# Optimization experiments

Hardware: AMD Instinct MI355X
Metric: run time of the kernel (lower is better)

The kernel has to match this reference:

```python
import jax, jax.numpy as jnp
import numpy as np

B, T, D = 128, 256, 1024  # batch, output_length (unroll steps), hidden size


def setup_inputs() -> dict:
    key = jax.random.key(0)
    k1, k2, k3 = jax.random.split(key, 3)
    scale = 0.02  # keep gates out of deep saturation
    return {
        "x": jax.random.normal(k1, (B, 1, D), dtype=jnp.float32),
        "kernel": jax.random.normal(k2, (D, 3 * D), dtype=jnp.float32) * scale,
        "rec_kernel": jax.random.normal(k3, (D, 3 * D), dtype=jnp.float32) * scale,
        "bias": jnp.zeros((3 * D,), dtype=jnp.float32),
        "output_length": T,
    }


def _gru_cell(x, h, kernel, rec_kernel, bias):
    # Classic GRU (Keras reset_after=False): gates from input and recurrent paths.
    gx = x @ kernel + bias            # [B, 3D]
    gh = h @ rec_kernel               # [B, 3D]
    xz, xr, xh = jnp.split(gx, 3, axis=-1)
    hz, hr, hh = jnp.split(gh, 3, axis=-1)
    z = jax.nn.sigmoid(xz + hz)       # update gate
    r = jax.nn.sigmoid(xr + hr)       # reset gate
    h_cand = jnp.tanh(xh + r * hh)
    return z * h + (1.0 - z) * h_cand


def reference(x, kernel, rec_kernel, bias, output_length):
    # RecursiveUnroll: feed the cell its own output, seeded by x, state init zeros.
    x0 = x[:, 0, :]                   # [B, D]
    h0 = jnp.zeros_like(x0)

    def step(carry, _):
        xt, ht = carry
        h_new = _gru_cell(xt, ht, kernel, rec_kernel, bias)
        # cell output == new state; it is both next input and next state
        return (h_new, h_new), h_new

    _, ys = jax.lax.scan(step, (x0, h0), None, length=output_length - 1)  # [T-1, B, D]
    out = jnp.concatenate([x0[None], ys], axis=0)  # [T, B, D]; first slot is the seed x
    return jnp.transpose(out, (1, 0, 2))           # [B, T, D]
```

## Files before the change

### kernel.cpp

```cpp
#include <hip/hip_runtime.h>
#include <hip/hip_bf16.h>

typedef short s16x8 __attribute__((ext_vector_type(8)));
typedef float f32x4 __attribute__((ext_vector_type(4)));

#define B_  128
#define T_  256
#define D_  1024

#define WPACK_BYTES (6144u * 2048u)
#define HBUF_BYTES  (128u * 1024u * 2u)
#define HA_OFF      (WPACK_BYTES)
#define HB_OFF      (HA_OFF + HBUF_BYTES)
#define SLOTS_OFF   (HB_OFF + HBUF_BYTES)
#define EPOCH_OFF   (SLOTS_OFF + 256u * 64u)
#define WS_NEEDED   (EPOCH_OFF + 8u * 64u)

static __device__ __forceinline__ float sigm_f(float x) {
  float e = __builtin_amdgcn_exp2f(-1.4426950408889634f * x);
  return __builtin_amdgcn_rcpf(1.0f + e);
}
static __device__ __forceinline__ float tanh_f(float x) {
  float e = __builtin_amdgcn_exp2f(-2.8853900817779268f * x);
  return 2.0f * __builtin_amdgcn_rcpf(1.0f + e) - 1.0f;
}
static __device__ __forceinline__ unsigned short f2bf(float f) {
  return __builtin_bit_cast(unsigned short, __float2bfloat16(f));
}
static __device__ __forceinline__ s16x8 ldg_coh(const char* p) {
  s16x8 v;
  asm volatile("global_load_dwordx4 %0, %1, off sc0 sc1" : "=v"(v) : "v"(p));
  return v;
}
static __device__ __forceinline__ void stg_coh(char* p, s16x8 v) {
  asm volatile("global_store_dwordx4 %0, %1, off sc0 sc1" :: "v"(p), "v"(v) : "memory");
}
static __device__ __forceinline__ unsigned hoff(int b, int k) {
  unsigned bb = (unsigned)b >> 6, mt = ((unsigned)b >> 4) & 3u, r = (unsigned)b & 15u;
  unsigned kk = (unsigned)k >> 5, g = ((unsigned)k >> 3) & 3u, k0 = (unsigned)k & 7u;
  return (((((bb * 32u + kk) * 4u + mt) * 4u + g) * 16u + r) * 8u + k0) * 2u;
}

extern "C" __global__ __launch_bounds__(256)
void gru_prepass(const float* __restrict__ x, const float* __restrict__ Wk,
                 const float* __restrict__ Wr, float* __restrict__ out,
                 char* __restrict__ ws) {
  const int W = blockIdx.x, tid = threadIdx.x;
  if (W < 3072) {
    const int v = W * 4 + (tid >> 6);
    const int lane = tid & 63;
    const int cb = v % 96, gk = v / 96;
    const int c = cb * 64 + lane;
    const float* src = (c < 3072) ? (Wk + c) : (Wr + (c - 3072));
    s16x8 pk;
#pragma unroll
    for (int j = 0; j < 8; ++j) {
      float val = src[(size_t)(gk * 8 + j) * 3072u];
      pk[j] = (short)f2bf(val);
    }
    *(s16x8*)(ws + (size_t)c * 2048u + (unsigned)gk * 16u) = pk;
  } else if (W < 3200) {
    const int b = W - 3072;
    const int k4 = tid * 4;
    float4 v = *(const float4*)(x + (size_t)b * D_ + k4);
    ushort4 u;
    u.x = f2bf(v.x); u.y = f2bf(v.y); u.z = f2bf(v.z); u.w = f2bf(v.w);
    *(ushort4*)(ws + HA_OFF + hoff(b, k4)) = u;
    *(float4*)(out + ((size_t)b * T_) * D_ + k4) = v;
  } else {
    if (tid < 256) *(unsigned*)(ws + SLOTS_OFF + (unsigned)tid * 64u) = 0u;
    if (tid < 8)   *(unsigned*)(ws + EPOCH_OFF + (unsigned)tid * 64u) = 0u;
  }
}

extern "C" __global__ __launch_bounds__(256, 1)
void gru_main(const float* __restrict__ bias, float* __restrict__ out,
              char* __restrict__ ws) {
  __shared__ f32x4 lds_red[4 * 3 * 64];
  __shared__ __align__(16) unsigned short stag[4 * 128];

  const int tid = threadIdx.x;
  const int w = tid >> 6, lane = tid & 63;
  const int bb = blockIdx.x >> 7;
  const int db = blockIdx.x & 127;
  const int d0 = db * 8, b0 = bb * 64;
  const int kh = w & 1;
  const int mh = w >> 1;

  char* hA = ws + HA_OFF;
  char* hB = ws + HB_OFF;
  unsigned* myslot = (unsigned*)(ws + SLOTS_OFF + (unsigned)blockIdx.x * 64u);

  s16x8 breg[3][16];
#pragma unroll
  for (int nt = 0; nt < 3; ++nt) {
    const int lc = nt * 16 + (lane & 15);
    const int c = (lc >> 3) * 1024 + d0 + (lc & 7);
    const char* colp = ws + (size_t)c * 2048u + (unsigned)((lane >> 4) * 16);
#pragma unroll
    for (int i = 0; i < 16; ++i) {
      const int kk = kh * 16 + i;
      breg[nt][i] = *(const s16x8*)(colp + (unsigned)kk * 64u);
    }
  }

  const int dl = lane & 7;
  const float bz = bias[d0 + dl];
  const float br = bias[1024 + d0 + dl];
  const float bh = bias[2048 + d0 + dl];
  const int hi = (lane >> 3) & 1;
  const int d = d0 + dl;
  const unsigned abase_off = (unsigned)(((bb * 32 + kh * 16) * 4) + mh * 2) * 1024u;
  const unsigned hbase = hoff(b0 + w * 16, d0);

  float hprev[4] = {0.f, 0.f, 0.f, 0.f};

  for (int t = 1; t < 256; ++t) {
    const char* hs = (t & 1) ? hA : hB;
    char*       hd = (t & 1) ? hB : hA;

    s16x8 areg0[16], areg1[16];
    {
      const char* ab = hs + abase_off + (unsigned)(lane * 16);
#pragma unroll
      for (int i = 0; i < 16; ++i) {
        areg0[i] = ldg_coh(ab);
        areg1[i] = ldg_coh(ab + 1024u);
        ab += 4096u;
      }
    }
    __builtin_amdgcn_sched_barrier(0);

    f32x4 acc0[3], acc1[3];
#pragma unroll
    for (int nt = 0; nt < 3; ++nt) {
      acc0[nt] = (f32x4){0.f, 0.f, 0.f, 0.f};
      acc1[nt] = (f32x4){0.f, 0.f, 0.f, 0.f};
    }

    asm volatile("s_waitcnt vmcnt(16)" ::: "memory");
    __builtin_amdgcn_sched_barrier(0);
#pragma unroll
    for (int i = 0; i < 8; ++i)
#pragma unroll
      for (int nt = 0; nt < 3; ++nt) {
        acc0[nt] = __builtin_amdgcn_mfma_f32_16x16x32_bf16(areg0[i], breg[nt][i], acc0[nt], 0, 0, 0);
        acc1[nt] = __builtin_amdgcn_mfma_f32_16x16x32_bf16(areg1[i], breg[nt][i], acc1[nt], 0, 0, 0);
      }
    asm volatile("s_waitcnt vmcnt(0)" ::: "memory");
    __builtin_amdgcn_sched_barrier(0);
#pragma unroll
    for (int i = 8; i < 16; ++i)
#pragma unroll
      for (int nt = 0; nt < 3; ++nt) {
        acc0[nt] = __builtin_amdgcn_mfma_f32_16x16x32_bf16(areg0[i], breg[nt][i], acc0[nt], 0, 0, 0);
        acc1[nt] = __builtin_amdgcn_mfma_f32_16x16x32_bf16(areg1[i], breg[nt][i], acc1[nt], 0, 0, 0);
      }

#pragma unroll
    for (int nt = 0; nt < 3; ++nt)
      lds_red[(w * 3 + nt) * 64 + lane] = (w & 1) ? acc0[nt] : acc1[nt];
    __syncthreads();
    f32x4 g3[3];
#pragma unroll
    for (int nt = 0; nt < 3; ++nt) {
      f32x4 mine = (w & 1) ? acc1[nt] : acc0[nt];
      g3[nt] = mine + lds_red[((w ^ 1) * 3 + nt) * 64 + lane];
    }

    float o0[4], o1[4], o2[4];
#pragma unroll
    for (int j = 0; j < 4; ++j) {
      o0[j] = __shfl_xor(g3[0][j], 8);
      o1[j] = __shfl_xor(g3[1][j], 8);
      o2[j] = __shfl_xor(g3[2][j], 8);
    }

    float hn_v[4];
#pragma unroll
    for (int j = 0; j < 4; ++j) {
      float xz = hi ? o0[j] : g3[0][j];
      float xh = hi ? o1[j] : g3[1][j];
      float hr = hi ? o2[j] : g3[2][j];
      float xr = hi ? g3[0][j] : o0[j];
      float hz = hi ? g3[1][j] : o1[j];
      float hh = hi ? g3[2][j] : o2[j];
      if (t == 1) { hz = 0.f; hr = 0.f; hh = 0.f; }
      float z  = sigm_f(xz + bz + hz);
      float r  = sigm_f(xr + br + hr);
      float hc = tanh_f(xh + bh + r * hh);
      float hn = z * hprev[j] + (1.f - z) * hc;
      hn_v[j] = hn;
      hprev[j] = hn;
      if (hi == 0)
        stag[w * 128 + ((lane >> 4) * 4 + j) * 8 + dl] = f2bf(hn);
    }

    __syncthreads();
    if (lane < 16) {
      s16x8 pk = *(const s16x8*)&stag[w * 128 + lane * 8];
      stg_coh(hd + hbase + (unsigned)(lane * 16), pk);
    }
    asm volatile("s_waitcnt vmcnt(0)" ::: "memory");
    __builtin_amdgcn_sched_barrier(0);
    __syncthreads();

    if (tid == 0)
      __hip_atomic_store(myslot, (unsigned)t, __ATOMIC_RELAXED, __HIP_MEMORY_SCOPE_AGENT);

    if (hi == 1) {
#pragma unroll
      for (int j = 0; j < 4; ++j) {
        const int brow = b0 + w * 16 + (lane >> 4) * 4 + j;
        __builtin_nontemporal_store(hn_v[j], &out[((size_t)brow * T_ + t) * D_ + d]);
      }
    }

    if (t == 255) break;

    if (blockIdx.x == 0 && w == 0) {
      int guard = 0;
      for (;;) {
        bool ok = true;
#pragma unroll
        for (int j = 0; j < 4; ++j) {
          unsigned s = __hip_atomic_load(
              (const unsigned*)(ws + SLOTS_OFF + (unsigned)(lane * 4 + j) * 64u),
              __ATOMIC_RELAXED, __HIP_MEMORY_SCOPE_AGENT);
          ok &= (s >= (unsigned)t);
        }
        if (__all(ok)) break;
        __builtin_amdgcn_s_sleep(1);
        if (++guard > (1 << 20)) break;
      }
      if (lane < 8)
        __hip_atomic_store((unsigned*)(ws + EPOCH_OFF + (unsigned)lane * 64u),
                           (unsigned)t, __ATOMIC_RELAXED, __HIP_MEMORY_SCOPE_AGENT);
    } else if (w == 0) {
      const unsigned* ep = (const unsigned*)(ws + EPOCH_OFF + (unsigned)((blockIdx.x >> 5) * 64));
      int guard = 0;
      while (__hip_atomic_load(ep, __ATOMIC_RELAXED, __HIP_MEMORY_SCOPE_AGENT)
             < (unsigned)t) {
        if (++guard > (1 << 22)) break;
      }
    }
    __syncthreads();
  }
}

extern "C" void kernel_launch(void* const* d_in, const int* in_sizes, int n_in,
                              void* d_out, int out_size, void* d_ws, size_t ws_size,
                              hipStream_t stream) {
  (void)in_sizes; (void)n_in; (void)out_size;
  if (ws_size < WS_NEEDED) return;
  const float* x    = (const float*)d_in[0];
  const float* Wk   = (const float*)d_in[1];
  const float* Wr   = (const float*)d_in[2];
  const float* bias = (const float*)d_in[3];
  float* out = (float*)d_out;
  char*  ws  = (char*)d_ws;

  hipLaunchKernelGGL(gru_prepass, dim3(3201), dim3(256), 0, stream, x, Wk, Wr, out, ws);
  hipLaunchKernelGGL(gru_main,    dim3(256),  dim3(256), 0, stream, bias, out, ws);
}
```

Measured before the change: 1.478 ms.

## Replace global barrier with per-team slot polling and stage hidden state through LDS

Blocks are regrouped into four independent teams of 64 blocks, each owning 32 batch rows and 16 hidden columns. The central master-block barrier with epoch flags is replaced by each block polling only its own team's 64 packed slot counters before loading the next step's state. The hidden-state layout is changed so that each team's 64 KB slice is read cooperatively into LDS once per block, and the waves then fetch their MFMA operands from LDS instead of issuing redundant coherent global loads. The aim is to shorten the per-step synchronization chain and cut global traffic. The cost is a 64 KB LDS footprint, extra __syncthreads, and slot counters packed into shared cache lines that all polling blocks contend on.

```diff
diff --git a/kernel.cpp b/kernel.cpp
--- a/kernel.cpp
+++ b/kernel.cpp
@@ -13,8 +13,7 @@
 #define HA_OFF      (WPACK_BYTES)
 #define HB_OFF      (HA_OFF + HBUF_BYTES)
 #define SLOTS_OFF   (HB_OFF + HBUF_BYTES)
-#define EPOCH_OFF   (SLOTS_OFF + 256u * 64u)
-#define WS_NEEDED   (EPOCH_OFF + 8u * 64u)
+#define WS_NEEDED   (SLOTS_OFF + 1024u)
 
 static __device__ __forceinline__ float sigm_f(float x) {
   float e = __builtin_amdgcn_exp2f(-1.4426950408889634f * x);
@@ -36,9 +35,9 @@
   asm volatile("global_store_dwordx4 %0, %1, off sc0 sc1" :: "v"(p), "v"(v) : "memory");
 }
 static __device__ __forceinline__ unsigned hoff(int b, int k) {
-  unsigned bb = (unsigned)b >> 6, mt = ((unsigned)b >> 4) & 3u, r = (unsigned)b & 15u;
-  unsigned kk = (unsigned)k >> 5, g = ((unsigned)k >> 3) & 3u, k0 = (unsigned)k & 7u;
-  return (((((bb * 32u + kk) * 4u + mt) * 4u + g) * 16u + r) * 8u + k0) * 2u;
+  unsigned rg = (unsigned)b >> 4, r = (unsigned)b & 15u;
+  unsigned kk = (unsigned)k >> 5, ks = ((unsigned)k >> 3) & 3u, k0 = (unsigned)k & 7u;
+  return (rg * 32u + kk) * 1024u + (ks * 16u + r) * 16u + k0 * 2u;
 }
 
 extern "C" __global__ __launch_bounds__(256)
@@ -68,34 +67,34 @@
     *(ushort4*)(ws + HA_OFF + hoff(b, k4)) = u;
     *(float4*)(out + ((size_t)b * T_) * D_ + k4) = v;
   } else {
-    if (tid < 256) *(unsigned*)(ws + SLOTS_OFF + (unsigned)tid * 64u) = 0u;
-    if (tid < 8)   *(unsigned*)(ws + EPOCH_OFF + (unsigned)tid * 64u) = 0u;
+    if (tid < 256) ((unsigned*)(ws + SLOTS_OFF))[tid] = 0u;
   }
 }
 
 extern "C" __global__ __launch_bounds__(256, 1)
 void gru_main(const float* __restrict__ bias, float* __restrict__ out,
               char* __restrict__ ws) {
-  __shared__ f32x4 lds_red[4 * 3 * 64];
-  __shared__ __align__(16) unsigned short stag[4 * 128];
+  __shared__ __align__(16) char ldsA[64 * 1024];
+  f32x4* lds_red = (f32x4*)ldsA;
+  unsigned short* stag = (unsigned short*)(ldsA + 12 * 1024);
 
   const int tid = threadIdx.x;
   const int w = tid >> 6, lane = tid & 63;
-  const int bb = blockIdx.x >> 7;
-  const int db = blockIdx.x & 127;
-  const int d0 = db * 8, b0 = bb * 64;
   const int kh = w & 1;
-  const int mh = w >> 1;
+  const int nh = w >> 1;
+  const int tau = blockIdx.x >> 6;
+  const int db  = blockIdx.x & 63;
+  const int d0w = db * 16 + nh * 8;
 
   char* hA = ws + HA_OFF;
   char* hB = ws + HB_OFF;
-  unsigned* myslot = (unsigned*)(ws + SLOTS_OFF + (unsigned)blockIdx.x * 64u);
+  unsigned* slots = (unsigned*)(ws + SLOTS_OFF);
 
   s16x8 breg[3][16];
 #pragma unroll
   for (int nt = 0; nt < 3; ++nt) {
     const int lc = nt * 16 + (lane & 15);
-    const int c = (lc >> 3) * 1024 + d0 + (lc & 7);
+    const int c = (lc >> 3) * 1024 + d0w + (lc & 7);
     const char* colp = ws + (size_t)c * 2048u + (unsigned)((lane >> 4) * 16);
 #pragma unroll
     for (int i = 0; i < 16; ++i) {
@@ -105,13 +104,14 @@
   }
 
   const int dl = lane & 7;
-  const float bz = bias[d0 + dl];
-  const float br = bias[1024 + d0 + dl];
-  const float bh = bias[2048 + d0 + dl];
+  const float bz = bias[d0w + dl];
+  const float br = bias[1024 + d0w + dl];
+  const float bh = bias[2048 + d0w + dl];
   const int hi = (lane >> 3) & 1;
-  const int d = d0 + dl;
-  const unsigned abase_off = (unsigned)(((bb * 32 + kh * 16) * 4) + mh * 2) * 1024u;
-  const unsigned hbase = hoff(b0 + w * 16, d0);
+  const int d = d0w + dl;
+  const unsigned teamA = (unsigned)tau * 65536u;
+  const unsigned hstore_off = teamA + (unsigned)(kh * 32 + (db >> 1)) * 1024u
+                            + (unsigned)(2 * (db & 1) + nh) * 256u;
 
   float hprev[4] = {0.f, 0.f, 0.f, 0.f};
 
@@ -119,52 +119,61 @@
     const char* hs = (t & 1) ? hA : hB;
     char*       hd = (t & 1) ? hB : hA;
 
-    s16x8 areg0[16], areg1[16];
+    if (t > 1) {
+      const unsigned* sl = slots + tau * 64 + lane;
+      int guard = 0;
+      while (!__all(__hip_atomic_load(sl, __ATOMIC_RELAXED, __HIP_MEMORY_SCOPE_AGENT)
+                    >= (unsigned)(t - 1))) {
+        __builtin_amdgcn_s_sleep(1);
+        if (++guard > (1 << 22)) break;
+      }
+    }
+
     {
-      const char* ab = hs + abase_off + (unsigned)(lane * 16);
+      s16x8 tmp[16];
+      const char* gb = hs + teamA + (unsigned)(w * 16) * 1024u + (unsigned)(lane * 16);
+#pragma unroll
+      for (int j = 0; j < 16; ++j) tmp[j] = ldg_coh(gb + (unsigned)j * 1024u);
+      asm volatile("s_waitcnt vmcnt(0)" ::: "memory");
+      __builtin_amdgcn_sched_barrier(0);
+      char* lb = ldsA + (unsigned)(w * 16) * 1024u + (unsigned)(lane * 16);
+#pragma unroll
+      for (int j = 0; j < 16; ++j) *(s16x8*)(lb + (unsigned)j * 1024u) = tmp[j];
+    }
+    __syncthreads();
+
+    s16x8 a0[16], a1[16];
+    {
+      const char* l0 = ldsA + (unsigned)(kh * 16) * 1024u + (unsigned)(lane * 16);
 #pragma unroll
       for (int i = 0; i < 16; ++i) {
-        areg0[i] = ldg_coh(ab);
-        areg1[i] = ldg_coh(ab + 1024u);
-        ab += 4096u;
-      }
-    }
-    __builtin_amdgcn_sched_barrier(0);
-
+        a0[i] = *(const s16x8*)(l0 + (unsigned)i * 1024u);
+        a1[i] = *(const s16x8*)(l0 + 32768u + (unsigned)i * 1024u);
+      }
+    }
     f32x4 acc0[3], acc1[3];
 #pragma unroll
     for (int nt = 0; nt < 3; ++nt) {
       acc0[nt] = (f32x4){0.f, 0.f, 0.f, 0.f};
       acc1[nt] = (f32x4){0.f, 0.f, 0.f, 0.f};
     }
-
-    asm volatile("s_waitcnt vmcnt(16)" ::: "memory");
-    __builtin_amdgcn_sched_barrier(0);
-#pragma unroll
-    for (int i = 0; i < 8; ++i)
+#pragma unroll
+    for (int i = 0; i < 16; ++i)
 #pragma unroll
       for (int nt = 0; nt < 3; ++nt) {
-        acc0[nt] = __builtin_amdgcn_mfma_f32_16x16x32_bf16(areg0[i], breg[nt][i], acc0[nt], 0, 0, 0);
-        acc1[nt] = __builtin_amdgcn_mfma_f32_16x16x32_bf16(areg1[i], breg[nt][i], acc1[nt], 0, 0, 0);
-      }
-    asm volatile("s_waitcnt vmcnt(0)" ::: "memory");
-    __builtin_amdgcn_sched_barrier(0);
-#pragma unroll
-    for (int i = 8; i < 16; ++i)
-#pragma unroll
-      for (int nt = 0; nt < 3; ++nt) {
-        acc0[nt] = __builtin_amdgcn_mfma_f32_16x16x32_bf16(areg0[i], breg[nt][i], acc0[nt], 0, 0, 0);
-        acc1[nt] = __builtin_amdgcn_mfma_f32_16x16x32_bf16(areg1[i], breg[nt][i], acc1[nt], 0, 0, 0);
-      }
+        acc0[nt] = __builtin_amdgcn_mfma_f32_16x16x32_bf16(a0[i], breg[nt][i], acc0[nt], 0, 0, 0);
+        acc1[nt] = __builtin_amdgcn_mfma_f32_16x16x32_bf16(a1[i], breg[nt][i], acc1[nt], 0, 0, 0);
+      }
+    __syncthreads();
 
 #pragma unroll
     for (int nt = 0; nt < 3; ++nt)
-      lds_red[(w * 3 + nt) * 64 + lane] = (w & 1) ? acc0[nt] : acc1[nt];
+      lds_red[(w * 3 + nt) * 64 + lane] = kh ? acc0[nt] : acc1[nt];
     __syncthreads();
     f32x4 g3[3];
 #pragma unroll
     for (int nt = 0; nt < 3; ++nt) {
-      f32x4 mine = (w & 1) ? acc1[nt] : acc0[nt];
+      f32x4 mine = kh ? acc1[nt] : acc0[nt];
       g3[nt] = mine + lds_red[((w ^ 1) * 3 + nt) * 64 + lane];
     }
 
@@ -196,55 +205,27 @@
         stag[w * 128 + ((lane >> 4) * 4 + j) * 8 + dl] = f2bf(hn);
     }
 
-    __syncthreads();
-    if (lane < 16) {
-      s16x8 pk = *(const s16x8*)&stag[w * 128 + lane * 8];
-      stg_coh(hd + hbase + (unsigned)(lane * 16), pk);
-    }
-    asm volatile("s_waitcnt vmcnt(0)" ::: "memory");
-    __builtin_amdgcn_sched_barrier(0);
-    __syncthreads();
-
-    if (tid == 0)
-      __hip_atomic_store(myslot, (unsigned)t, __ATOMIC_RELAXED, __HIP_MEMORY_SCOPE_AGENT);
+    if (t < 255) {
+      __syncthreads();
+      if (lane < 16) {
+        s16x8 pk = *(const s16x8*)&stag[w * 128 + lane * 8];
+        stg_coh(hd + hstore_off + (unsigned)(lane * 16), pk);
+      }
+      asm volatile("s_waitcnt vmcnt(0)" ::: "memory");
+      __builtin_amdgcn_sched_barrier(0);
+      __syncthreads();
+      if (tid == 0)
+        __hip_atomic_store(&slots[blockIdx.x], (unsigned)t,
+                           __ATOMIC_RELAXED, __HIP_MEMORY_SCOPE_AGENT);
+    }
 
     if (hi == 1) {
 #pragma unroll
       for (int j = 0; j < 4; ++j) {
-        const int brow = b0 + w * 16 + (lane >> 4) * 4 + j;
+        const int brow = tau * 32 + kh * 16 + (lane >> 4) * 4 + j;
         __builtin_nontemporal_store(hn_v[j], &out[((size_t)brow * T_ + t) * D_ + d]);
       }
     }
-
-    if (t == 255) break;
-
-    if (blockIdx.x == 0 && w == 0) {
-      int guard = 0;
-      for (;;) {
-        bool ok = true;
-#pragma unroll
-        for (int j = 0; j < 4; ++j) {
-          unsigned s = __hip_atomic_load(
-              (const unsigned*)(ws + SLOTS_OFF + (unsigned)(lane * 4 + j) * 64u),
-              __ATOMIC_RELAXED, __HIP_MEMORY_SCOPE_AGENT);
-          ok &= (s >= (unsigned)t);
-        }
-        if (__all(ok)) break;
-        __builtin_amdgcn_s_sleep(1);
-        if (++guard > (1 << 20)) break;
-      }
-      if (lane < 8)
-        __hip_atomic_store((unsigned*)(ws + EPOCH_OFF + (unsigned)lane * 64u),
-                           (unsigned)t, __ATOMIC_RELAXED, __HIP_MEMORY_SCOPE_AGENT);
-    } else if (w == 0) {
-      const unsigned* ep = (const unsigned*)(ws + EPOCH_OFF + (unsigned)((blockIdx.x >> 5) * 64));
-      int guard = 0;
-      while (__hip_atomic_load(ep, __ATOMIC_RELAXED, __HIP_MEMORY_SCOPE_AGENT)
-             < (unsigned)t) {
-        if (++guard > (1 << 22)) break;
-      }
-    }
-    __syncthreads();
   }
 }
 
```

Result: slower. 1.630 ms (+10.3%).
